# Kernel tuning notes

Measured on AMD Instinct MI355X. Metric: run time of the kernel, lower is better.

The kernel has to match this reference:

```python
import jax, jax.numpy as jnp
import numpy as np

N = 50000      # nodes
E = 1600000    # edges (avg degree 32)
F_IN = 3       # PROTEINS num_node_features
H = 64         # dim_h
G = 512        # num graphs in batch
C = 2          # PROTEINS num_classes
BN_EPS = 1e-5


def setup_inputs() -> dict:
    key = jax.random.key(0)
    ks = iter(jax.random.split(key, 64))

    def rn(shape, s=0.1):
        return (jax.random.normal(next(ks), shape) * s).astype(jnp.float32)

    inp = {"x": rn((N, F_IN), 1.0)}
    for li, din in ((1, F_IN), (2, H), (3, H)):
        p = f"conv{li}_"
        inp[p + "w1"] = rn((din, H))
        inp[p + "b1"] = rn((H,))
        inp[p + "bn_g"] = jnp.ones((H,), jnp.float32)
        inp[p + "bn_b"] = jnp.zeros((H,), jnp.float32)
        inp[p + "bn_m"] = rn((H,))
        inp[p + "bn_v"] = jax.random.uniform(next(ks), (H,), jnp.float32, 0.5, 1.5)
        inp[p + "w2"] = rn((H, H))
        inp[p + "b2"] = rn((H,))
    inp["lin1_w"] = rn((3 * H, 3 * H))
    inp["lin1_b"] = rn((3 * H,))
    inp["lin2_w"] = rn((3 * H, C))
    inp["lin2_b"] = rn((C,))
    inp["edge_index"] = jax.random.randint(next(ks), (2, E), 0, N, jnp.int64)
    inp["batch"] = jnp.sort(jax.random.randint(next(ks), (N,), 0, G, jnp.int64))
    return inp


def gin_conv(x, src, dst, w1, b1, g, bb, m, v, w2, b2):
    # GINConv, eps=0: mlp(x + sum_{j->i} x_j); aggregate messages at target (dst)
    agg = jax.ops.segment_sum(x[src], dst, num_segments=N)  # [N, d]
    h = x + agg
    h = h @ w1 + b1
    h = (h - m) * jax.lax.rsqrt(v + BN_EPS) * g + bb  # BatchNorm1d (eval)
    h = jax.nn.relu(h)
    h = jax.nn.relu(h @ w2 + b2)
    return h


def reference(x,
              conv1_w1, conv1_b1, conv1_bn_g, conv1_bn_b, conv1_bn_m, conv1_bn_v, conv1_w2, conv1_b2,
              conv2_w1, conv2_b1, conv2_bn_g, conv2_bn_b, conv2_bn_m, conv2_bn_v, conv2_w2, conv2_b2,
              conv3_w1, conv3_b1, conv3_bn_g, conv3_bn_b, conv3_bn_m, conv3_bn_v, conv3_w2, conv3_b2,
              lin1_w, lin1_b, lin2_w, lin2_b,
              edge_index, batch):
    src, dst = edge_index[0], edge_index[1]
    h1 = gin_conv(x,  src, dst, conv1_w1, conv1_b1, conv1_bn_g, conv1_bn_b, conv1_bn_m, conv1_bn_v, conv1_w2, conv1_b2)
    h2 = gin_conv(h1, src, dst, conv2_w1, conv2_b1, conv2_bn_g, conv2_bn_b, conv2_bn_m, conv2_bn_v, conv2_w2, conv2_b2)
    h3 = gin_conv(h2, src, dst, conv3_w1, conv3_b1, conv3_bn_g, conv3_bn_b, conv3_bn_m, conv3_bn_v, conv3_w2, conv3_b2)
    # global_add_pool per graph
    p1 = jax.ops.segment_sum(h1, batch, num_segments=G)
    p2 = jax.ops.segment_sum(h2, batch, num_segments=G)
    p3 = jax.ops.segment_sum(h3, batch, num_segments=G)
    h = jnp.concatenate((p1, p2, p3), axis=1)          # [G, 3H]
    h = jax.nn.relu(h @ lin1_w + lin1_b)
    # dropout p=0.5 is identity in eval mode
    h = h @ lin2_w + lin2_b                            # [G, C]
    return (h, jax.nn.log_softmax(h, axis=1))
```

## Files before the change

### kernel.cpp

```cpp
#include <hip/hip_runtime.h>
#include <hip/hip_bf16.h>
#include <math.h>

#define N_NODES 50000
#define N_EDGES 1600000
#define H 64
#define G_GRAPHS 512
#define C_CLS 2
#define BN_EPS 1e-5f
#define NBUCK 196
#define BUCKCAP 16384
#define E4 (N_EDGES / 4)
#define CSR_BLOCKS ((E4 + 511) / 512)
#define IOP 72

typedef __attribute__((ext_vector_type(8))) short short8;
typedef __attribute__((ext_vector_type(4))) float floatx4;

__device__ __forceinline__ float bflo(unsigned int u) { return __uint_as_float(u << 16); }
__device__ __forceinline__ float bfhi(unsigned int u) { return __uint_as_float(u & 0xffff0000u); }
__device__ __forceinline__ unsigned int bf16_rne(float f) {
    unsigned int u = __float_as_uint(f);
    u += 0x7fffu + ((u >> 16) & 1u);
    return u >> 16;
}

__global__ __launch_bounds__(256) void prep_kernel(
    const float* __restrict__ w2_0, const float* __restrict__ w1_1,
    const float* __restrict__ w2_1, const float* __restrict__ w1_2,
    const float* __restrict__ w2_2, unsigned short* __restrict__ wt,
    const float* __restrict__ x, uint2* __restrict__ xb) {
    int b = blockIdx.x, t = threadIdx.x;
    if (b < 5) {
        const float* w = (b == 0) ? w2_0 : (b == 1) ? w1_1 : (b == 2) ? w2_1
                         : (b == 3) ? w1_2 : w2_2;
        unsigned short* o = wt + b * (H * H);
        for (int idx = t; idx < H * H; idx += 256) {
            int k = idx >> 6, j = idx & 63;
            o[j * H + k] = (unsigned short)bf16_rne(w[idx]);
        }
    } else {
        int node = (b - 5) * 256 + t;
        if (node < N_NODES) {
            uint2 p;
            p.x = bf16_rne(x[node * 3 + 0]) | (bf16_rne(x[node * 3 + 1]) << 16);
            p.y = bf16_rne(x[node * 3 + 2]);
            xb[node] = p;
        }
    }
}

__global__ __launch_bounds__(256) void scatter1_kernel(const int* __restrict__ src,
                                                       const int* __restrict__ dst,
                                                       int* __restrict__ gcnt,
                                                       int* __restrict__ gpacked) {
    __shared__ int bh[NBUCK];
    int t = threadIdx.x;
    if (t < NBUCK) bh[t] = 0;
    __syncthreads();
    int base = blockIdx.x * 512;

    int pkA[4], bkA[4], lrA[4]; bool vA = false;
    int pkB[4], bkB[4], lrB[4]; bool vB = false;
    {
        int i = base + t;
        if (i < E4) {
            vA = true;
            int4 s4 = ((const int4*)src)[i];
            int4 d4 = ((const int4*)dst)[i];
            bkA[0] = d4.x >> 8; pkA[0] = ((d4.x & 255) << 16) | s4.x; lrA[0] = atomicAdd(&bh[bkA[0]], 1);
            bkA[1] = d4.y >> 8; pkA[1] = ((d4.y & 255) << 16) | s4.y; lrA[1] = atomicAdd(&bh[bkA[1]], 1);
            bkA[2] = d4.z >> 8; pkA[2] = ((d4.z & 255) << 16) | s4.z; lrA[2] = atomicAdd(&bh[bkA[2]], 1);
            bkA[3] = d4.w >> 8; pkA[3] = ((d4.w & 255) << 16) | s4.w; lrA[3] = atomicAdd(&bh[bkA[3]], 1);
        }
    }
    {
        int i = base + 256 + t;
        if (i < E4) {
            vB = true;
            int4 s4 = ((const int4*)src)[i];
            int4 d4 = ((const int4*)dst)[i];
            bkB[0] = d4.x >> 8; pkB[0] = ((d4.x & 255) << 16) | s4.x; lrB[0] = atomicAdd(&bh[bkB[0]], 1);
            bkB[1] = d4.y >> 8; pkB[1] = ((d4.y & 255) << 16) | s4.y; lrB[1] = atomicAdd(&bh[bkB[1]], 1);
            bkB[2] = d4.z >> 8; pkB[2] = ((d4.z & 255) << 16) | s4.z; lrB[2] = atomicAdd(&bh[bkB[2]], 1);
            bkB[3] = d4.w >> 8; pkB[3] = ((d4.w & 255) << 16) | s4.w; lrB[3] = atomicAdd(&bh[bkB[3]], 1);
        }
    }
    __syncthreads();
    if (t < NBUCK) {
        int c = bh[t];
        bh[t] = c ? atomicAdd(&gcnt[t], c) : 0;
    }
    __syncthreads();
    if (vA) {
#pragma unroll
        for (int q = 0; q < 4; q++) gpacked[bkA[q] * BUCKCAP + bh[bkA[q]] + lrA[q]] = pkA[q];
    }
    if (vB) {
#pragma unroll
        for (int q = 0; q < 4; q++) gpacked[bkB[q] * BUCKCAP + bh[bkB[q]] + lrB[q]] = pkB[q];
    }
}

__global__ __launch_bounds__(256) void bcsr_kernel(const int* __restrict__ gpacked,
                                                   const int* __restrict__ gcnt,
                                                   int* __restrict__ row_start,
                                                   int* __restrict__ edge_src) {
    __shared__ int cnt[256];
    __shared__ int pref[256];
    int b = blockIdx.x;
    int t = threadIdx.x;

    int v = (t < NBUCK) ? gcnt[t] : 0;
    pref[t] = v;
    __syncthreads();
    for (int off = 1; off < 256; off <<= 1) {
        int u = 0;
        if (t >= off) u = pref[t - off];
        __syncthreads();
        if (t >= off) pref[t] += u;
        __syncthreads();
    }
    int bs = (b > 0) ? pref[b - 1] : 0;
    int cnt_b = gcnt[b];
    if (b == 0 && t == 0) row_start[N_NODES] = N_EDGES;
    __syncthreads();

    const int* gp = gpacked + (size_t)b * BUCKCAP;
    cnt[t] = 0;
    __syncthreads();
    for (int i = t; i < cnt_b; i += 256) atomicAdd(&cnt[gp[i] >> 16], 1);
    __syncthreads();
    int c = cnt[t];
    pref[t] = c;
    __syncthreads();
    for (int off = 1; off < 256; off <<= 1) {
        int u = 0;
        if (t >= off) u = pref[t - off];
        __syncthreads();
        if (t >= off) pref[t] += u;
        __syncthreads();
    }
    int excl = pref[t] - c;
    int node = b * 256 + t;
    if (node < N_NODES) row_start[node] = bs + excl;
    cnt[t] = excl;
    __syncthreads();
    for (int i = t; i < cnt_b; i += 256) {
        int p = gp[i];
        int pos = atomicAdd(&cnt[p >> 16], 1);
        edge_src[bs + pos] = p & 0xffff;
    }
}

__global__ __launch_bounds__(512) void gin1_fused16_kernel(
    const float* __restrict__ x, const uint2* __restrict__ xb,
    const int* __restrict__ row_start, const int* __restrict__ edge_src,
    const float* __restrict__ w1, const float* __restrict__ b1,
    const float* __restrict__ bn_g, const float* __restrict__ bn_b,
    const float* __restrict__ bn_m, const float* __restrict__ bn_v,
    const unsigned short* __restrict__ w2t, const float* __restrict__ b2,
    __hip_bfloat16* __restrict__ hout) {
    __shared__ unsigned short s_mid[16 * IOP];

    int tid = threadIdx.x;
    int wave = tid >> 6, j = tid & 63;
    int nodebase = blockIdx.x * 16;

    float wj0 = w1[j], wj1 = w1[H + j], wj2 = w1[2 * H + j];
    float sc = rsqrtf(bn_v[j] + BN_EPS) * bn_g[j];
    float sh = bn_b[j] - bn_m[j] * sc;
    float bj = b1[j];

    for (int nl = wave * 2; nl < wave * 2 + 2; nl++) {
        int node = nodebase + nl;
        int rs = row_start[node], re = row_start[node + 1];
        float a0 = 0.f, a1 = 0.f, a2 = 0.f;
        for (int t = rs + j; t < re; t += 64) {
            uint2 p = xb[edge_src[t]];
            a0 += bflo(p.x); a1 += bfhi(p.x); a2 += bflo(p.y);
        }
#pragma unroll
        for (int off = 32; off > 0; off >>= 1) {
            a0 += __shfl_xor(a0, off);
            a1 += __shfl_xor(a1, off);
            a2 += __shfl_xor(a2, off);
        }
        float in0 = a0 + x[node * 3 + 0];
        float in1 = a1 + x[node * 3 + 1];
        float in2 = a2 + x[node * 3 + 2];
        float m = bj + in0 * wj0 + in1 * wj1 + in2 * wj2;
        m = fmaxf(m * sc + sh, 0.f);
        s_mid[nl * IOP + j] = (unsigned short)bf16_rne(m);
    }
    __syncthreads();

    if (wave == 0) {
        int quad = j >> 4, l15 = j & 15;
        float bb2[4];
#pragma unroll
        for (int jt = 0; jt < 4; jt++) bb2[jt] = b2[jt * 16 + l15];

        short8 m0 = *(const short8*)&s_mid[l15 * IOP + quad * 8];
        short8 m1 = *(const short8*)&s_mid[l15 * IOP + quad * 8 + 32];
#pragma unroll
        for (int jt = 0; jt < 4; jt++) {
            short8 b0 = *(const short8*)&w2t[(jt * 16 + l15) * H + quad * 8];
            short8 bv = *(const short8*)&w2t[(jt * 16 + l15) * H + quad * 8 + 32];
            floatx4 c = {0.f, 0.f, 0.f, 0.f};
            c = __builtin_amdgcn_mfma_f32_16x16x32_bf16(m0, b0, c, 0, 0, 0);
            c = __builtin_amdgcn_mfma_f32_16x16x32_bf16(m1, bv, c, 0, 0, 0);
#pragma unroll
            for (int r = 0; r < 4; r++) {
                float v = fmaxf(c[r] + bb2[jt], 0.f);
                s_mid[(quad * 4 + r) * IOP + jt * 16 + l15] = (unsigned short)bf16_rne(v);
            }
        }
        unsigned short* ho = (unsigned short*)hout;
#pragma unroll
        for (int cc = 0; cc < 2; cc++) {
            int r = cc * 8 + (j >> 3);
            short8 v = *(const short8*)&s_mid[r * IOP + (j & 7) * 8];
            *(short8*)(ho + (size_t)(nodebase + r) * H + (j & 7) * 8) = v;
        }
    }
}

__global__ __launch_bounds__(512) void gin_fused16_kernel(
    const __hip_bfloat16* __restrict__ hin, const int* __restrict__ row_start,
    const int* __restrict__ edge_src,
    const unsigned short* __restrict__ w1t, const float* __restrict__ b1,
    const float* __restrict__ bn_g, const float* __restrict__ bn_b,
    const float* __restrict__ bn_m, const float* __restrict__ bn_v,
    const unsigned short* __restrict__ w2t, const float* __restrict__ b2,
    __hip_bfloat16* __restrict__ hout) {
    __shared__ unsigned short s_xs[16 * IOP];
    __shared__ unsigned short s_mid[16 * IOP];

    int tid = threadIdx.x;
    int wave = tid >> 6, j = tid & 63;
    int o = j >> 3, jo = j & 7;
    int nodebase = blockIdx.x * 16;

    const char* hb = (const char*)hin;

    for (int nl = wave * 2; nl < wave * 2 + 2; nl++) {
        int node = nodebase + nl;
        int rs = row_start[node], re = row_start[node + 1];
        float a0 = 0.f, a1 = 0.f, a2 = 0.f, a3 = 0.f, a4 = 0.f, a5 = 0.f, a6 = 0.f, a7 = 0.f;
        float b0 = 0.f, b1v = 0.f, b2v = 0.f, b3 = 0.f, b4 = 0.f, b5 = 0.f, b6 = 0.f, b7 = 0.f;
        for (int base = rs; base < re; base += 64) {
            int idx = base + j;
            int sv = (idx < re) ? edge_src[idx] : 0;
            int cnt = min(64, re - base);
            int i = 0;
            for (; i + 16 <= cnt; i += 16) {
                int s0 = __shfl(sv, i + o);
                int s1 = __shfl(sv, i + 8 + o);
                uint4 r0 = *(const uint4*)(hb + (size_t)s0 * 128 + jo * 16);
                uint4 r1 = *(const uint4*)(hb + (size_t)s1 * 128 + jo * 16);
                a0 += bflo(r0.x); a1 += bfhi(r0.x);
                a2 += bflo(r0.y); a3 += bfhi(r0.y);
                a4 += bflo(r0.z); a5 += bfhi(r0.z);
                a6 += bflo(r0.w); a7 += bfhi(r0.w);
                b0 += bflo(r1.x); b1v += bfhi(r1.x);
                b2v += bflo(r1.y); b3 += bfhi(r1.y);
                b4 += bflo(r1.z); b5 += bfhi(r1.z);
                b6 += bflo(r1.w); b7 += bfhi(r1.w);
            }
            for (; i + 8 <= cnt; i += 8) {
                int s = __shfl(sv, i + o);
                uint4 raw = *(const uint4*)(hb + (size_t)s * 128 + jo * 16);
                a0 += bflo(raw.x); a1 += bfhi(raw.x);
                a2 += bflo(raw.y); a3 += bfhi(raw.y);
                a4 += bflo(raw.z); a5 += bfhi(raw.z);
                a6 += bflo(raw.w); a7 += bfhi(raw.w);
            }
            if (i < cnt) {
                int r = cnt - i;
                int s = __shfl(sv, i + (o < r ? o : 0));
                uint4 raw = *(const uint4*)(hb + (size_t)s * 128 + jo * 16);
                if (o < r) {
                    a0 += bflo(raw.x); a1 += bfhi(raw.x);
                    a2 += bflo(raw.y); a3 += bfhi(raw.y);
                    a4 += bflo(raw.z); a5 += bfhi(raw.z);
                    a6 += bflo(raw.w); a7 += bfhi(raw.w);
                }
            }
        }
        a0 += b0; a1 += b1v; a2 += b2v; a3 += b3;
        a4 += b4; a5 += b5; a6 += b6; a7 += b7;
        a0 += __shfl_xor(a0, 8); a0 += __shfl_xor(a0, 16); a0 += __shfl_xor(a0, 32);
        a1 += __shfl_xor(a1, 8); a1 += __shfl_xor(a1, 16); a1 += __shfl_xor(a1, 32);
        a2 += __shfl_xor(a2, 8); a2 += __shfl_xor(a2, 16); a2 += __shfl_xor(a2, 32);
        a3 += __shfl_xor(a3, 8); a3 += __shfl_xor(a3, 16); a3 += __shfl_xor(a3, 32);
        a4 += __shfl_xor(a4, 8); a4 += __shfl_xor(a4, 16); a4 += __shfl_xor(a4, 32);
        a5 += __shfl_xor(a5, 8); a5 += __shfl_xor(a5, 16); a5 += __shfl_xor(a5, 32);
        a6 += __shfl_xor(a6, 8); a6 += __shfl_xor(a6, 16); a6 += __shfl_xor(a6, 32);
        a7 += __shfl_xor(a7, 8); a7 += __shfl_xor(a7, 16); a7 += __shfl_xor(a7, 32);
        if (o == 0) {
            uint4 raw = *(const uint4*)(hb + (size_t)node * 128 + jo * 16);
            a0 += bflo(raw.x); a1 += bfhi(raw.x);
            a2 += bflo(raw.y); a3 += bfhi(raw.y);
            a4 += bflo(raw.z); a5 += bfhi(raw.z);
            a6 += bflo(raw.w); a7 += bfhi(raw.w);
            uint4 ov;
            ov.x = bf16_rne(a0) | (bf16_rne(a1) << 16);
            ov.y = bf16_rne(a2) | (bf16_rne(a3) << 16);
            ov.z = bf16_rne(a4) | (bf16_rne(a5) << 16);
            ov.w = bf16_rne(a6) | (bf16_rne(a7) << 16);
            *(uint4*)&s_xs[nl * IOP + jo * 8] = ov;
        }
    }
    __syncthreads();

    if (wave == 0) {
        int quad = j >> 4, l15 = j & 15;
        float scl[4], sht[4], bb1[4], bb2[4];
#pragma unroll
        for (int jt = 0; jt < 4; jt++) {
            int jj = jt * 16 + l15;
            float sc = rsqrtf(bn_v[jj] + BN_EPS) * bn_g[jj];
            scl[jt] = sc;
            sht[jt] = bn_b[jj] - bn_m[jj] * sc;
            bb1[jt] = b1[jj];
            bb2[jt] = b2[jj];
        }
        short8 a0 = *(const short8*)&s_xs[l15 * IOP + quad * 8];
        short8 a1 = *(const short8*)&s_xs[l15 * IOP + quad * 8 + 32];
#pragma unroll
        for (int jt = 0; jt < 4; jt++) {
            short8 b0 = *(const short8*)&w1t[(jt * 16 + l15) * H + quad * 8];
            short8 bv = *(const short8*)&w1t[(jt * 16 + l15) * H + quad * 8 + 32];
            floatx4 c = {0.f, 0.f, 0.f, 0.f};
            c = __builtin_amdgcn_mfma_f32_16x16x32_bf16(a0, b0, c, 0, 0, 0);
            c = __builtin_amdgcn_mfma_f32_16x16x32_bf16(a1, bv, c, 0, 0, 0);
#pragma unroll
            for (int r = 0; r < 4; r++) {
                float v = (c[r] + bb1[jt]) * scl[jt] + sht[jt];
                v = fmaxf(v, 0.f);
                s_mid[(quad * 4 + r) * IOP + jt * 16 + l15] = (unsigned short)bf16_rne(v);
            }
        }
        short8 m0 = *(const short8*)&s_mid[l15 * IOP + quad * 8];
        short8 m1 = *(const short8*)&s_mid[l15 * IOP + quad * 8 + 32];
#pragma unroll
        for (int jt = 0; jt < 4; jt++) {
            short8 b0 = *(const short8*)&w2t[(jt * 16 + l15) * H + quad * 8];
            short8 bv = *(const short8*)&w2t[(jt * 16 + l15) * H + quad * 8 + 32];
            floatx4 c = {0.f, 0.f, 0.f, 0.f};
            c = __builtin_amdgcn_mfma_f32_16x16x32_bf16(m0, b0, c, 0, 0, 0);
            c = __builtin_amdgcn_mfma_f32_16x16x32_bf16(m1, bv, c, 0, 0, 0);
#pragma unroll
            for (int r = 0; r < 4; r++) {
                float v = fmaxf(c[r] + bb2[jt], 0.f);
                s_xs[(quad * 4 + r) * IOP + jt * 16 + l15] = (unsigned short)bf16_rne(v);
            }
        }
        unsigned short* ho = (unsigned short*)hout;
#pragma unroll
        for (int cc = 0; cc < 2; cc++) {
            int r = cc * 8 + (j >> 3);
            short8 v = *(const short8*)&s_xs[r * IOP + (j & 7) * 8];
            *(short8*)(ho + (size_t)(nodebase + r) * H + (j & 7) * 8) = v;
        }
    }
}

__global__ __launch_bounds__(192) void pool_head_kernel(
    const __hip_bfloat16* __restrict__ h1, const __hip_bfloat16* __restrict__ h2,
    const __hip_bfloat16* __restrict__ h3, const int* __restrict__ batch,
    const float* __restrict__ lin1_w, const float* __restrict__ lin1_b,
    const float* __restrict__ lin2_w, const float* __restrict__ lin2_b,
    float* __restrict__ out) {
    __shared__ float s_row[3 * H];
    __shared__ float s_mid[3 * H];
    __shared__ float s_z[C_CLS];
    __shared__ int s_se[2];

    int g = blockIdx.x;
    int j = threadIdx.x;
    if (j < 2) {
        int target = g + j;
        int lo = 0, hi = N_NODES;
        while (lo < hi) {
            int mid = (lo + hi) >> 1;
            if (batch[mid] < target) lo = mid + 1; else hi = mid;
        }
        s_se[j] = lo;
    }
    __syncthreads();
    int ns = s_se[0], ne = s_se[1];

    int which = j >> 6;
    int f = j & 63;
    const __hip_bfloat16* h = (which == 0) ? h1 : ((which == 1) ? h2 : h3);
    float p0 = 0.f, p1 = 0.f, p2 = 0.f, p3 = 0.f;
    int n = ns;
    for (; n + 3 < ne; n += 4) {
        p0 += __bfloat162float(h[(size_t)n * H + f]);
        p1 += __bfloat162float(h[(size_t)(n + 1) * H + f]);
        p2 += __bfloat162float(h[(size_t)(n + 2) * H + f]);
        p3 += __bfloat162float(h[(size_t)(n + 3) * H + f]);
    }
    for (; n < ne; n++) p0 += __bfloat162float(h[(size_t)n * H + f]);
    s_row[j] = (p0 + p1) + (p2 + p3);
    __syncthreads();

    float acc = lin1_b[j];
    for (int k = 0; k < 3 * H; k++) acc += s_row[k] * lin1_w[k * (3 * H) + j];
    s_mid[j] = fmaxf(acc, 0.f);
    __syncthreads();

    if (j < C_CLS) {
        float z = lin2_b[j];
        for (int k = 0; k < 3 * H; k++) z += s_mid[k] * lin2_w[k * C_CLS + j];
        s_z[j] = z;
    }
    __syncthreads();
    if (j < C_CLS) {
        float z0 = s_z[0], z1 = s_z[1];
        float mx = fmaxf(z0, z1);
        float lse = mx + logf(expf(z0 - mx) + expf(z1 - mx));
        out[g * C_CLS + j] = s_z[j];
        out[G_GRAPHS * C_CLS + g * C_CLS + j] = s_z[j] - lse;
    }
}

extern "C" void kernel_launch(void* const* d_in, const int* in_sizes, int n_in,
                              void* d_out, int out_size, void* d_ws, size_t ws_size,
                              hipStream_t stream) {
    const float* x = (const float*)d_in[0];
    const float* cw1[3], *cb1[3], *cg[3], *cbb[3], *cm[3], *cv[3], *cw2[3], *cb2[3];
    for (int l = 0; l < 3; l++) {
        int b = 1 + 8 * l;
        cw1[l] = (const float*)d_in[b + 0];
        cb1[l] = (const float*)d_in[b + 1];
        cg[l]  = (const float*)d_in[b + 2];
        cbb[l] = (const float*)d_in[b + 3];
        cm[l]  = (const float*)d_in[b + 4];
        cv[l]  = (const float*)d_in[b + 5];
        cw2[l] = (const float*)d_in[b + 6];
        cb2[l] = (const float*)d_in[b + 7];
    }
    const float* lin1_w = (const float*)d_in[25];
    const float* lin1_b = (const float*)d_in[26];
    const float* lin2_w = (const float*)d_in[27];
    const float* lin2_b = (const float*)d_in[28];
    const int* edge_index = (const int*)d_in[29];
    const int* batch = (const int*)d_in[30];
    const int* src = edge_index;
    const int* dst = edge_index + N_EDGES;
    float* out = (float*)d_out;

    int* edge_src = (int*)d_ws;
    int* gpacked = edge_src + N_EDGES;
    int* gcnt = gpacked + (size_t)NBUCK * BUCKCAP;
    int* row_start = gcnt + NBUCK;
    uintptr_t hp = (uintptr_t)(row_start + N_NODES + 2);
    hp = (hp + 127) & ~(uintptr_t)127;
    unsigned short* wt = (unsigned short*)hp;
    uint2* xb = (uint2*)(wt + 5 * H * H);
    __hip_bfloat16* h1 = (__hip_bfloat16*)(xb + N_NODES);
    __hip_bfloat16* h2 = h1 + (size_t)N_NODES * H;
    __hip_bfloat16* h3 = h2 + (size_t)N_NODES * H;

    const unsigned short* w2t_0 = wt + 0 * H * H;
    const unsigned short* w1t_1 = wt + 1 * H * H;
    const unsigned short* w2t_1 = wt + 2 * H * H;
    const unsigned short* w1t_2 = wt + 3 * H * H;
    const unsigned short* w2t_2 = wt + 4 * H * H;

    hipMemsetAsync(gcnt, 0, NBUCK * sizeof(int), stream);
    prep_kernel<<<5 + (N_NODES + 255) / 256, 256, 0, stream>>>(
        cw2[0], cw1[1], cw2[1], cw1[2], cw2[2], wt, x, xb);
    scatter1_kernel<<<CSR_BLOCKS, 256, 0, stream>>>(src, dst, gcnt, gpacked);
    bcsr_kernel<<<NBUCK, 256, 0, stream>>>(gpacked, gcnt, row_start, edge_src);

    const int fgrid = N_NODES / 16;

    gin1_fused16_kernel<<<fgrid, 512, 0, stream>>>(x, xb, row_start, edge_src,
        cw1[0], cb1[0], cg[0], cbb[0], cm[0], cv[0], w2t_0, cb2[0], h1);
    gin_fused16_kernel<<<fgrid, 512, 0, stream>>>(h1, row_start, edge_src,
        w1t_1, cb1[1], cg[1], cbb[1], cm[1], cv[1], w2t_1, cb2[1], h2);
    gin_fused16_kernel<<<fgrid, 512, 0, stream>>>(h2, row_start, edge_src,
        w1t_2, cb1[2], cg[2], cbb[2], cm[2], cv[2], w2t_2, cb2[2], h3);
    pool_head_kernel<<<G_GRAPHS, 3 * H, 0, stream>>>(h1, h2, h3, batch,
        lin1_w, lin1_b, lin2_w, lin2_b, out);
}
```

Before: 281.9 us.

## Fuse global add pooling into GIN conv epilogues and merge prep with scatter

Each GIN layer kernel now atomically accumulates its fp32 post-ReLU outputs into a per-graph pool buffer. When a node quad shares one graph id, the four values are summed first and added with a single atomic. The pool/head kernel no longer binary-searches the batch array or rereads h1/h2/h3; it just loads the pooled row. The prep and bucket-scatter kernels are merged into one launch, and the memset is extended to zero the pool. This removes a pass over the hidden activations and one launch, at the cost of many global float atomics and non-deterministic summation order.

```diff
diff --git a/kernel.cpp b/kernel.cpp
--- a/kernel.cpp
+++ b/kernel.cpp
@@ -11,7 +11,8 @@
 #define NBUCK 196
 #define BUCKCAP 16384
 #define E4 (N_EDGES / 4)
-#define CSR_BLOCKS ((E4 + 511) / 512)
+#define SCHUNKS ((E4 + 511) / 512)
+#define XCHUNKS ((N_NODES + 255) / 256)
 #define IOP 72
 
 typedef __attribute__((ext_vector_type(8))) short short8;
@@ -25,80 +26,76 @@
     return u >> 16;
 }
 
-__global__ __launch_bounds__(256) void prep_kernel(
+__global__ __launch_bounds__(256) void prepscatter_kernel(
+    const int* __restrict__ src, const int* __restrict__ dst,
+    int* __restrict__ gcnt, int* __restrict__ gpacked,
     const float* __restrict__ w2_0, const float* __restrict__ w1_1,
     const float* __restrict__ w2_1, const float* __restrict__ w1_2,
     const float* __restrict__ w2_2, unsigned short* __restrict__ wt,
     const float* __restrict__ x, uint2* __restrict__ xb) {
     int b = blockIdx.x, t = threadIdx.x;
-    if (b < 5) {
-        const float* w = (b == 0) ? w2_0 : (b == 1) ? w1_1 : (b == 2) ? w2_1
-                         : (b == 3) ? w1_2 : w2_2;
-        unsigned short* o = wt + b * (H * H);
+    if (b < SCHUNKS) {
+        __shared__ int bh[NBUCK];
+        if (t < NBUCK) bh[t] = 0;
+        __syncthreads();
+        int base = b * 512;
+        int pkA[4], bkA[4], lrA[4]; bool vA = false;
+        int pkB[4], bkB[4], lrB[4]; bool vB = false;
+        {
+            int i = base + t;
+            if (i < E4) {
+                vA = true;
+                int4 s4 = ((const int4*)src)[i];
+                int4 d4 = ((const int4*)dst)[i];
+                bkA[0] = d4.x >> 8; pkA[0] = ((d4.x & 255) << 16) | s4.x; lrA[0] = atomicAdd(&bh[bkA[0]], 1);
+                bkA[1] = d4.y >> 8; pkA[1] = ((d4.y & 255) << 16) | s4.y; lrA[1] = atomicAdd(&bh[bkA[1]], 1);
+                bkA[2] = d4.z >> 8; pkA[2] = ((d4.z & 255) << 16) | s4.z; lrA[2] = atomicAdd(&bh[bkA[2]], 1);
+                bkA[3] = d4.w >> 8; pkA[3] = ((d4.w & 255) << 16) | s4.w; lrA[3] = atomicAdd(&bh[bkA[3]], 1);
+            }
+        }
+        {
+            int i = base + 256 + t;
+            if (i < E4) {
+                vB = true;
+                int4 s4 = ((const int4*)src)[i];
+                int4 d4 = ((const int4*)dst)[i];
+                bkB[0] = d4.x >> 8; pkB[0] = ((d4.x & 255) << 16) | s4.x; lrB[0] = atomicAdd(&bh[bkB[0]], 1);
+                bkB[1] = d4.y >> 8; pkB[1] = ((d4.y & 255) << 16) | s4.y; lrB[1] = atomicAdd(&bh[bkB[1]], 1);
+                bkB[2] = d4.z >> 8; pkB[2] = ((d4.z & 255) << 16) | s4.z; lrB[2] = atomicAdd(&bh[bkB[2]], 1);
+                bkB[3] = d4.w >> 8; pkB[3] = ((d4.w & 255) << 16) | s4.w; lrB[3] = atomicAdd(&bh[bkB[3]], 1);
+            }
+        }
+        __syncthreads();
+        if (t < NBUCK) {
+            int c = bh[t];
+            bh[t] = c ? atomicAdd(&gcnt[t], c) : 0;
+        }
+        __syncthreads();
+        if (vA) {
+#pragma unroll
+            for (int q = 0; q < 4; q++) gpacked[bkA[q] * BUCKCAP + bh[bkA[q]] + lrA[q]] = pkA[q];
+        }
+        if (vB) {
+#pragma unroll
+            for (int q = 0; q < 4; q++) gpacked[bkB[q] * BUCKCAP + bh[bkB[q]] + lrB[q]] = pkB[q];
+        }
+    } else if (b < SCHUNKS + 5) {
+        int w_id = b - SCHUNKS;
+        const float* w = (w_id == 0) ? w2_0 : (w_id == 1) ? w1_1 : (w_id == 2) ? w2_1
+                         : (w_id == 3) ? w1_2 : w2_2;
+        unsigned short* o = wt + w_id * (H * H);
         for (int idx = t; idx < H * H; idx += 256) {
-            int k = idx >> 6, j = idx & 63;
-            o[j * H + k] = (unsigned short)bf16_rne(w[idx]);
+            int k = idx >> 6, jc = idx & 63;
+            o[jc * H + k] = (unsigned short)bf16_rne(w[idx]);
         }
     } else {
-        int node = (b - 5) * 256 + t;
+        int node = (b - SCHUNKS - 5) * 256 + t;
         if (node < N_NODES) {
             uint2 p;
             p.x = bf16_rne(x[node * 3 + 0]) | (bf16_rne(x[node * 3 + 1]) << 16);
             p.y = bf16_rne(x[node * 3 + 2]);
             xb[node] = p;
         }
-    }
-}
-
-__global__ __launch_bounds__(256) void scatter1_kernel(const int* __restrict__ src,
-                                                       const int* __restrict__ dst,
-                                                       int* __restrict__ gcnt,
-                                                       int* __restrict__ gpacked) {
-    __shared__ int bh[NBUCK];
-    int t = threadIdx.x;
-    if (t < NBUCK) bh[t] = 0;
-    __syncthreads();
-    int base = blockIdx.x * 512;
-
-    int pkA[4], bkA[4], lrA[4]; bool vA = false;
-    int pkB[4], bkB[4], lrB[4]; bool vB = false;
-    {
-        int i = base + t;
-        if (i < E4) {
-            vA = true;
-            int4 s4 = ((const int4*)src)[i];
-            int4 d4 = ((const int4*)dst)[i];
-            bkA[0] = d4.x >> 8; pkA[0] = ((d4.x & 255) << 16) | s4.x; lrA[0] = atomicAdd(&bh[bkA[0]], 1);
-            bkA[1] = d4.y >> 8; pkA[1] = ((d4.y & 255) << 16) | s4.y; lrA[1] = atomicAdd(&bh[bkA[1]], 1);
-            bkA[2] = d4.z >> 8; pkA[2] = ((d4.z & 255) << 16) | s4.z; lrA[2] = atomicAdd(&bh[bkA[2]], 1);
-            bkA[3] = d4.w >> 8; pkA[3] = ((d4.w & 255) << 16) | s4.w; lrA[3] = atomicAdd(&bh[bkA[3]], 1);
-        }
-    }
-    {
-        int i = base + 256 + t;
-        if (i < E4) {
-            vB = true;
-            int4 s4 = ((const int4*)src)[i];
-            int4 d4 = ((const int4*)dst)[i];
-            bkB[0] = d4.x >> 8; pkB[0] = ((d4.x & 255) << 16) | s4.x; lrB[0] = atomicAdd(&bh[bkB[0]], 1);
-            bkB[1] = d4.y >> 8; pkB[1] = ((d4.y & 255) << 16) | s4.y; lrB[1] = atomicAdd(&bh[bkB[1]], 1);
-            bkB[2] = d4.z >> 8; pkB[2] = ((d4.z & 255) << 16) | s4.z; lrB[2] = atomicAdd(&bh[bkB[2]], 1);
-            bkB[3] = d4.w >> 8; pkB[3] = ((d4.w & 255) << 16) | s4.w; lrB[3] = atomicAdd(&bh[bkB[3]], 1);
-        }
-    }
-    __syncthreads();
-    if (t < NBUCK) {
-        int c = bh[t];
-        bh[t] = c ? atomicAdd(&gcnt[t], c) : 0;
-    }
-    __syncthreads();
-    if (vA) {
-#pragma unroll
-        for (int q = 0; q < 4; q++) gpacked[bkA[q] * BUCKCAP + bh[bkA[q]] + lrA[q]] = pkA[q];
-    }
-    if (vB) {
-#pragma unroll
-        for (int q = 0; q < 4; q++) gpacked[bkB[q] * BUCKCAP + bh[bkB[q]] + lrB[q]] = pkB[q];
     }
 }
 
@@ -160,12 +157,15 @@
     const float* __restrict__ bn_g, const float* __restrict__ bn_b,
     const float* __restrict__ bn_m, const float* __restrict__ bn_v,
     const unsigned short* __restrict__ w2t, const float* __restrict__ b2,
-    __hip_bfloat16* __restrict__ hout) {
+    __hip_bfloat16* __restrict__ hout, const int* __restrict__ batch,
+    float* __restrict__ pool) {
     __shared__ unsigned short s_mid[16 * IOP];
+    __shared__ int s_bat[16];
 
     int tid = threadIdx.x;
     int wave = tid >> 6, j = tid & 63;
     int nodebase = blockIdx.x * 16;
+    if (tid < 16) s_bat[tid] = batch[nodebase + tid];
 
     float wj0 = w1[j], wj1 = w1[H + j], wj2 = w1[2 * H + j];
     float sc = rsqrtf(bn_v[j] + BN_EPS) * bn_g[j];
@@ -176,8 +176,8 @@
         int node = nodebase + nl;
         int rs = row_start[node], re = row_start[node + 1];
         float a0 = 0.f, a1 = 0.f, a2 = 0.f;
-        for (int t = rs + j; t < re; t += 64) {
-            uint2 p = xb[edge_src[t]];
+        for (int t2 = rs + j; t2 < re; t2 += 64) {
+            uint2 p = xb[edge_src[t2]];
             a0 += bflo(p.x); a1 += bfhi(p.x); a2 += bflo(p.y);
         }
 #pragma unroll
@@ -203,6 +203,7 @@
 
         short8 m0 = *(const short8*)&s_mid[l15 * IOP + quad * 8];
         short8 m1 = *(const short8*)&s_mid[l15 * IOP + quad * 8 + 32];
+        int bq0 = s_bat[quad * 4], bq3 = s_bat[quad * 4 + 3];
 #pragma unroll
         for (int jt = 0; jt < 4; jt++) {
             short8 b0 = *(const short8*)&w2t[(jt * 16 + l15) * H + quad * 8];
@@ -210,10 +211,21 @@
             floatx4 c = {0.f, 0.f, 0.f, 0.f};
             c = __builtin_amdgcn_mfma_f32_16x16x32_bf16(m0, b0, c, 0, 0, 0);
             c = __builtin_amdgcn_mfma_f32_16x16x32_bf16(m1, bv, c, 0, 0, 0);
+            float vv[4];
 #pragma unroll
             for (int r = 0; r < 4; r++) {
                 float v = fmaxf(c[r] + bb2[jt], 0.f);
+                vv[r] = v;
                 s_mid[(quad * 4 + r) * IOP + jt * 16 + l15] = (unsigned short)bf16_rne(v);
+            }
+            int jj = jt * 16 + l15;
+            if (bq0 == bq3) {
+                atomicAdd(&pool[bq0 * 192 + jj], (vv[0] + vv[1]) + (vv[2] + vv[3]));
+            } else {
+                atomicAdd(&pool[s_bat[quad * 4 + 0] * 192 + jj], vv[0]);
+                atomicAdd(&pool[s_bat[quad * 4 + 1] * 192 + jj], vv[1]);
+                atomicAdd(&pool[s_bat[quad * 4 + 2] * 192 + jj], vv[2]);
+                atomicAdd(&pool[s_bat[quad * 4 + 3] * 192 + jj], vv[3]);
             }
         }
         unsigned short* ho = (unsigned short*)hout;
@@ -233,14 +245,17 @@
     const float* __restrict__ bn_g, const float* __restrict__ bn_b,
     const float* __restrict__ bn_m, const float* __restrict__ bn_v,
     const unsigned short* __restrict__ w2t, const float* __restrict__ b2,
-    __hip_bfloat16* __restrict__ hout) {
+    __hip_bfloat16* __restrict__ hout, const int* __restrict__ batch,
+    float* __restrict__ pool) {
     __shared__ unsigned short s_xs[16 * IOP];
     __shared__ unsigned short s_mid[16 * IOP];
+    __shared__ int s_bat[16];
 
     int tid = threadIdx.x;
     int wave = tid >> 6, j = tid & 63;
     int o = j >> 3, jo = j & 7;
     int nodebase = blockIdx.x * 16;
+    if (tid < 16) s_bat[tid] = batch[nodebase + tid];
 
     const char* hb = (const char*)hin;
 
@@ -344,6 +359,7 @@
         }
         short8 m0 = *(const short8*)&s_mid[l15 * IOP + quad * 8];
         short8 m1 = *(const short8*)&s_mid[l15 * IOP + quad * 8 + 32];
+        int bq0 = s_bat[quad * 4], bq3 = s_bat[quad * 4 + 3];
 #pragma unroll
         for (int jt = 0; jt < 4; jt++) {
             short8 b0 = *(const short8*)&w2t[(jt * 16 + l15) * H + quad * 8];
@@ -351,10 +367,21 @@
             floatx4 c = {0.f, 0.f, 0.f, 0.f};
             c = __builtin_amdgcn_mfma_f32_16x16x32_bf16(m0, b0, c, 0, 0, 0);
             c = __builtin_amdgcn_mfma_f32_16x16x32_bf16(m1, bv, c, 0, 0, 0);
+            float vv[4];
 #pragma unroll
             for (int r = 0; r < 4; r++) {
                 float v = fmaxf(c[r] + bb2[jt], 0.f);
+                vv[r] = v;
                 s_xs[(quad * 4 + r) * IOP + jt * 16 + l15] = (unsigned short)bf16_rne(v);
+            }
+            int jj = jt * 16 + l15;
+            if (bq0 == bq3) {
+                atomicAdd(&pool[bq0 * 192 + jj], (vv[0] + vv[1]) + (vv[2] + vv[3]));
+            } else {
+                atomicAdd(&pool[s_bat[quad * 4 + 0] * 192 + jj], vv[0]);
+                atomicAdd(&pool[s_bat[quad * 4 + 1] * 192 + jj], vv[1]);
+                atomicAdd(&pool[s_bat[quad * 4 + 2] * 192 + jj], vv[2]);
+                atomicAdd(&pool[s_bat[quad * 4 + 3] * 192 + jj], vv[3]);
             }
         }
         unsigned short* ho = (unsigned short*)hout;
@@ -367,44 +394,18 @@
     }
 }
 
-__global__ __launch_bounds__(192) void pool_head_kernel(
-    const __hip_bfloat16* __restrict__ h1, const __hip_bfloat16* __restrict__ h2,
-    const __hip_bfloat16* __restrict__ h3, const int* __restrict__ batch,
+__global__ __launch_bounds__(192) void head_kernel(
+    const float* __restrict__ pool,
     const float* __restrict__ lin1_w, const float* __restrict__ lin1_b,
     const float* __restrict__ lin2_w, const float* __restrict__ lin2_b,
     float* __restrict__ out) {
     __shared__ float s_row[3 * H];
     __shared__ float s_mid[3 * H];
     __shared__ float s_z[C_CLS];
-    __shared__ int s_se[2];
 
     int g = blockIdx.x;
     int j = threadIdx.x;
-    if (j < 2) {
-        int target = g + j;
-        int lo = 0, hi = N_NODES;
-        while (lo < hi) {
-            int mid = (lo + hi) >> 1;
-            if (batch[mid] < target) lo = mid + 1; else hi = mid;
-        }
-        s_se[j] = lo;
-    }
-    __syncthreads();
-    int ns = s_se[0], ne = s_se[1];
-
-    int which = j >> 6;
-    int f = j & 63;
-    const __hip_bfloat16* h = (which == 0) ? h1 : ((which == 1) ? h2 : h3);
-    float p0 = 0.f, p1 = 0.f, p2 = 0.f, p3 = 0.f;
-    int n = ns;
-    for (; n + 3 < ne; n += 4) {
-        p0 += __bfloat162float(h[(size_t)n * H + f]);
-        p1 += __bfloat162float(h[(size_t)(n + 1) * H + f]);
-        p2 += __bfloat162float(h[(size_t)(n + 2) * H + f]);
-        p3 += __bfloat162float(h[(size_t)(n + 3) * H + f]);
-    }
-    for (; n < ne; n++) p0 += __bfloat162float(h[(size_t)n * H + f]);
-    s_row[j] = (p0 + p1) + (p2 + p3);
+    s_row[j] = pool[g * 192 + j];
     __syncthreads();
 
     float acc = lin1_b[j];
@@ -456,7 +457,8 @@
     int* edge_src = (int*)d_ws;
     int* gpacked = edge_src + N_EDGES;
     int* gcnt = gpacked + (size_t)NBUCK * BUCKCAP;
-    int* row_start = gcnt + NBUCK;
+    float* pool = (float*)(gcnt + NBUCK);
+    int* row_start = (int*)(pool + G_GRAPHS * 3 * H);
     uintptr_t hp = (uintptr_t)(row_start + N_NODES + 2);
     hp = (hp + 127) & ~(uintptr_t)127;
     unsigned short* wt = (unsigned short*)hp;
@@ -471,20 +473,20 @@
     const unsigned short* w1t_2 = wt + 3 * H * H;
     const unsigned short* w2t_2 = wt + 4 * H * H;
 
-    hipMemsetAsync(gcnt, 0, NBUCK * sizeof(int), stream);
-    prep_kernel<<<5 + (N_NODES + 255) / 256, 256, 0, stream>>>(
-        cw2[0], cw1[1], cw2[1], cw1[2], cw2[2], wt, x, xb);
-    scatter1_kernel<<<CSR_BLOCKS, 256, 0, stream>>>(src, dst, gcnt, gpacked);
+    hipMemsetAsync(gcnt, 0, NBUCK * sizeof(int) + (size_t)G_GRAPHS * 3 * H * sizeof(float),
+                   stream);
+    prepscatter_kernel<<<SCHUNKS + 5 + XCHUNKS, 256, 0, stream>>>(
+        src, dst, gcnt, gpacked, cw2[0], cw1[1], cw2[1], cw1[2], cw2[2], wt, x, xb);
     bcsr_kernel<<<NBUCK, 256, 0, stream>>>(gpacked, gcnt, row_start, edge_src);
 
     const int fgrid = N_NODES / 16;
 
     gin1_fused16_kernel<<<fgrid, 512, 0, stream>>>(x, xb, row_start, edge_src,
-        cw1[0], cb1[0], cg[0], cbb[0], cm[0], cv[0], w2t_0, cb2[0], h1);
+        cw1[0], cb1[0], cg[0], cbb[0], cm[0], cv[0], w2t_0, cb2[0], h1, batch, pool);
     gin_fused16_kernel<<<fgrid, 512, 0, stream>>>(h1, row_start, edge_src,
-        w1t_1, cb1[1], cg[1], cbb[1], cm[1], cv[1], w2t_1, cb2[1], h2);
+        w1t_1, cb1[1], cg[1], cbb[1], cm[1], cv[1], w2t_1, cb2[1], h2, batch, pool + 64);
     gin_fused16_kernel<<<fgrid, 512, 0, stream>>>(h2, row_start, edge_src,
-        w1t_2, cb1[2], cg[2], cbb[2], cm[2], cv[2], w2t_2, cb2[2], h3);
-    pool_head_kernel<<<G_GRAPHS, 3 * H, 0, stream>>>(h1, h2, h3, batch,
+        w1t_2, cb1[2], cg[2], cbb[2], cm[2], cv[2], w2t_2, cb2[2], h3, batch, pool + 128);
+    head_kernel<<<G_GRAPHS, 3 * H, 0, stream>>>(pool,
         lin1_w, lin1_b, lin2_w, lin2_b, out);
 }
```

New measurement: 305.9 us. +8.5%, slower.
